# Kernel tuning notes

Measured on AMD Instinct MI355X. Metric: run time of the kernel, lower is better.

Reference implementation:

```python
import jax, jax.numpy as jnp
import numpy as np

PF = 16      # PATCH_FEATURES
PFD = 16     # PATCH_FEATURES_DEEP
NCLS = 10

def setup_inputs() -> dict:
    key = jax.random.key(0)
    ks = jax.random.split(key, 7)
    B = 131072
    x = jax.random.normal(ks[0], (B, 1, 28, 28), dtype=jnp.float32)
    # Linear params: W stored as [out, in] like torch, scaled kaiming-uniform-ish
    W1 = jax.random.uniform(ks[1], (PF, 49), jnp.float32, -1, 1) / jnp.sqrt(49.0)
    b1 = jax.random.uniform(ks[2], (PF,), jnp.float32, -1, 1) / jnp.sqrt(49.0)
    W2 = jax.random.uniform(ks[3], (PFD, 4 * PF), jnp.float32, -1, 1) / jnp.sqrt(64.0)
    b2 = jax.random.uniform(ks[4], (PFD,), jnp.float32, -1, 1) / jnp.sqrt(64.0)
    W3 = jax.random.uniform(ks[5], (NCLS, 4 * PFD), jnp.float32, -1, 1) / jnp.sqrt(64.0)
    b3 = jax.random.uniform(ks[6], (NCLS,), jnp.float32, -1, 1) / jnp.sqrt(64.0)
    return {"x": x, "W1": W1, "b1": b1, "W2": W2, "b2": b2, "W3": W3, "b3": b3}


def reference(x, W1, b1, W2, b2, W3, b3):
    # Dropout layers are identity in eval/inference mode.
    B = x.shape[0]
    img = x[:, 0]  # [B,28,28]
    # 16 non-overlapping 7x7 patches, flattened row-major (matches the torch slices)
    p = img.reshape(B, 4, 7, 4, 7).transpose(0, 1, 3, 2, 4).reshape(B, 4, 4, 49)
    # fc1 applied to every patch: one batched GEMM instead of 16 launches
    h = jnp.einsum('bijp,fp->bijf', p, W1) + b1          # [B,4,4,16]
    # group 2x2 patch blocks; concat order (x11,x12,x21,x22) = row-major (ii,jj)
    hb = h.reshape(B, 2, 2, 2, 2, PF).transpose(0, 1, 3, 2, 4, 5).reshape(B, 2, 2, 4 * PF)
    y = jnp.einsum('bijp,fp->bijf', hb, W2) + b2         # [B,2,2,16]
    # concat (y11,y12,y21,y22) row-major over (bi,bj), relu, fc3
    yflat = jax.nn.relu(y).reshape(B, 4 * PFD)           # [B,64]
    z = yflat @ W3.T + b3                                # [B,10]
    return jax.nn.log_softmax(z, axis=1)
```

## Files before the change

### kernel.cpp

```cpp
#include <hip/hip_runtime.h>

typedef float f32x4 __attribute__((ext_vector_type(4)));
typedef short bf16x8 __attribute__((ext_vector_type(8)));

#define XS 464
#define WOFF 29696
#define YOFF 29696
#define YS 144
#define BOFF 38912

__device__ __forceinline__ unsigned short f2bf(float f) {
  unsigned u = __builtin_bit_cast(unsigned, f);
  u += 0x7FFFu + ((u >> 16) & 1u);
  return (unsigned short)(u >> 16);
}
__device__ __forceinline__ unsigned packbf2(float a, float b) {
  return (unsigned)f2bf(a) | ((unsigned)f2bf(b) << 16);
}

__global__ __launch_bounds__(256, 2) void mnist_mfma(
    const float* __restrict__ x, const float* __restrict__ W1,
    const float* __restrict__ b1, const float* __restrict__ W2,
    const float* __restrict__ b2, const float* __restrict__ W3,
    const float* __restrict__ b3, float* __restrict__ out, int nimg)
{
  __shared__ __align__(16) char smem[38976];
  float* smemF = (float*)smem;
  const int tid = threadIdx.x;
  const int lane = tid & 63;
  const int waveid = tid >> 6;

  for (int i = tid; i < 784; i += 256) smemF[i] = W1[i];
  for (int i = tid; i < 1024; i += 256) smemF[784 + i] = W2[i];
  __syncthreads();

  unsigned short* w12b = (unsigned short*)(smem + WOFF);
  for (int e = tid; e < 3136; e += 256) {
    int f2 = e / 196, k = e - f2 * 196;
    int r14 = k / 14, c14 = k - r14 * 14;
    int pp = (r14 % 7) * 7 + (c14 % 7);
    int q = (r14 / 7) * 2 + (c14 / 7);
    float s = 0.f;
#pragma unroll
    for (int f = 0; f < 16; ++f)
      s = fmaf(smemF[f * 49 + pp], smemF[784 + f2 * 64 + q * 16 + f], s);
    w12b[f2 * 232 + k] = f2bf(s);
  }
  for (int e = tid; e < 576; e += 256) {
    int f2 = e / 36;
    w12b[f2 * 232 + 196 + (e - f2 * 36)] = 0;
  }
  if (tid < 16) {
    float s = b2[tid];
#pragma unroll
    for (int k = 0; k < 64; ++k)
      s = fmaf(b1[k & 15], smemF[784 + tid * 64 + k], s);
    smemF[BOFF / 4 + tid] = s;
  }
  __syncthreads();

  bf16x8 wfrag[7];
#pragma unroll
  for (int i = 0; i < 7; ++i)
    wfrag[i] = *(const bf16x8*)(smem + WOFF + (lane & 15) * XS + (lane >> 4) * 16 + i * 64);

  bf16x8 w3f[2];
  {
    int o = lane & 15, kb = (lane >> 4) * 8;
#pragma unroll
    for (int mi = 0; mi < 2; ++mi) {
      float v[8];
#pragma unroll
      for (int j = 0; j < 8; ++j)
        v[j] = (o < 10) ? W3[o * 64 + kb + 32 * mi + j] : 0.f;
      unsigned t[4];
      t[0] = packbf2(v[0], v[1]); t[1] = packbf2(v[2], v[3]);
      t[2] = packbf2(v[4], v[5]); t[3] = packbf2(v[6], v[7]);
      w3f[mi] = __builtin_bit_cast(bf16x8, *(unsigned(*)[4])t);
    }
  }
  const float b12v = smemF[BOFF / 4 + (lane & 15)];
  float b3v[4];
#pragma unroll
  for (int r = 0; r < 4; ++r) {
    int o = (lane >> 4) * 4 + r;
    b3v[r] = (o < 10) ? b3[o] : 0.f;
  }
  __syncthreads();

  char* xw = smem + waveid * 7424;
#pragma unroll
  for (int j = 0; j < 5; ++j) {
    int idx = lane + 64 * j;
    if (idx < 288) {
      int row = idx / 18, d = idx - row * 18;
      *(unsigned*)(xw + row * XS + 392 + d * 4) = 0;
    }
  }

  unsigned wa0[13]; unsigned strm = 0;
#pragma unroll
  for (int it = 0; it < 13; ++it) {
    int gi = lane + 64 * it;
    int im = gi / 196, rem = gi - im * 196;
    int rr = rem / 7, t = rem - rr * 7;
    int c2 = 2 * t;
    int J = c2 / 7, cq = c2 - 7 * J;
    int row = im * 4 + (rr / 14) * 2 + J;
    int kp = (rr % 14) * 7 + cq;
    wa0[it] = waveid * 7424 + row * XS + kp * 4;
    if (t == 3) strm |= (1u << it);
  }

  const unsigned xrd = waveid * 7424 + (lane & 15) * XS + (lane >> 4) * 16;
  const unsigned ywb = YOFF + waveid * 2304 + (lane & 15) * 2;
  const unsigned yrd = YOFF + waveid * 2304 + (lane & 15) * YS + (lane >> 4) * 16;

  const int NU = nimg >> 4;
  const int WST = (int)(gridDim.x << 2);
  const int w0 = (int)(blockIdx.x << 2) + waveid;
  const int ng4 = nimg >> 2;

  f32x4 cur[13];
  const f32x4* __restrict__ xq0 = (const f32x4*)x;
  auto issue4 = [&](int g4) {
    const f32x4* p = xq0 + (size_t)g4 * 784;
#pragma unroll
    for (int it = 0; it < 12; ++it)
      cur[it] = __builtin_nontemporal_load(p + lane + 64 * it);
    if (lane < 16) cur[12] = __builtin_nontemporal_load(p + 768 + lane);
  };

  if (w0 < NU) issue4(w0 * 4);

  for (int u = w0; u < NU; u += WST) {
#pragma unroll 1
    for (int sb = 0; sb < 4; ++sb) {
#pragma unroll
      for (int it = 0; it < 13; ++it) {
        if (it == 12 && lane >= 16) continue;
        f32x4 v = cur[it];
        unsigned a0 = wa0[it];
        unsigned d = ((strm >> it) & 1) ? 440u : 4u;
        *(unsigned*)(smem + a0) = packbf2(v.x, v.y);
        *(unsigned*)(smem + a0 + d) = packbf2(v.z, v.w);
      }
      int ng = (sb < 3) ? (u * 4 + sb + 1) : ((u + WST) * 4);
      if (ng < ng4) issue4(ng);
      f32x4 acc = {0.f, 0.f, 0.f, 0.f};
#pragma unroll
      for (int i = 0; i < 7; ++i) {
        bf16x8 a = *(const bf16x8*)(smem + xrd + 64 * i);
        acc = __builtin_amdgcn_mfma_f32_16x16x32_bf16(a, wfrag[i], acc, 0, 0, 0);
      }
      unsigned yb = ywb + (unsigned)(sb * 4 + (lane >> 4)) * YS;
#pragma unroll
      for (int r = 0; r < 4; ++r) {
        float yv = fmaxf(acc[r] + b12v, 0.f);
        *(unsigned short*)(smem + yb + r * 32) = f2bf(yv);
      }
    }
    f32x4 z4 = {0.f, 0.f, 0.f, 0.f};
#pragma unroll
    for (int mi = 0; mi < 2; ++mi) {
      bf16x8 bfr = *(const bf16x8*)(smem + yrd + 64 * mi);
      z4 = __builtin_amdgcn_mfma_f32_16x16x32_bf16(w3f[mi], bfr, z4, 0, 0, 0);
    }
    float zv[4], mval = -3.0e38f;
#pragma unroll
    for (int r = 0; r < 4; ++r) {
      zv[r] = z4[r] + b3v[r];
      bool valid = ((lane >> 4) * 4 + r) < 10;
      mval = fmaxf(mval, valid ? zv[r] : -3.0e38f);
    }
    mval = fmaxf(mval, __shfl_xor(mval, 16, 64));
    mval = fmaxf(mval, __shfl_xor(mval, 32, 64));
    float ssum = 0.f;
#pragma unroll
    for (int r = 0; r < 4; ++r) {
      bool valid = ((lane >> 4) * 4 + r) < 10;
      ssum += valid ? __expf(zv[r] - mval) : 0.f;
    }
    ssum += __shfl_xor(ssum, 16, 64);
    ssum += __shfl_xor(ssum, 32, 64);
    const float lse = mval + __logf(ssum);
    float* op = out + (size_t)(u * 16 + (lane & 15)) * 10;
#pragma unroll
    for (int r = 0; r < 4; ++r) {
      int o = (lane >> 4) * 4 + r;
      if (o < 10) op[o] = zv[r] - lse;
    }
  }
}

extern "C" void kernel_launch(void* const* d_in, const int* in_sizes, int n_in,
                              void* d_out, int out_size, void* d_ws, size_t ws_size,
                              hipStream_t stream) {
  const float* x  = (const float*)d_in[0];
  const float* W1 = (const float*)d_in[1];
  const float* b1 = (const float*)d_in[2];
  const float* W2 = (const float*)d_in[3];
  const float* b2 = (const float*)d_in[4];
  const float* W3 = (const float*)d_in[5];
  const float* b3 = (const float*)d_in[6];
  float* out = (float*)d_out;

  const int nimg = in_sizes[0] / 784;
  mnist_mfma<<<1024, 256, 0, stream>>>(x, W1, b1, W2, b2, W3, b3, out, nimg);
}
```

Before: 75.13 us.

## Double-buffer global image loads in registers to deepen the prefetch

Adds a second register buffer for input tiles, so two image groups' loads are in flight while the current group is staged to LDS and run through the MFMA. The loop is unrolled over two units per stride, alternating between the A and B buffers, and the next-next group is issued after each stage. The min-blocks hint is dropped from the launch bounds so the compiler can use the extra VGPRs. The intent is to hide more HBM latency in this bandwidth-bound kernel, at the cost of more registers and possibly lower occupancy.

```diff
diff --git a/kernel.cpp b/kernel.cpp
--- a/kernel.cpp
+++ b/kernel.cpp
@@ -18,7 +18,7 @@
   return (unsigned)f2bf(a) | ((unsigned)f2bf(b) << 16);
 }
 
-__global__ __launch_bounds__(256, 2) void mnist_mfma(
+__global__ __launch_bounds__(256) void mnist_mfma(
     const float* __restrict__ x, const float* __restrict__ W1,
     const float* __restrict__ b1, const float* __restrict__ W2,
     const float* __restrict__ b2, const float* __restrict__ W3,
@@ -119,47 +119,42 @@
   const int NU = nimg >> 4;
   const int WST = (int)(gridDim.x << 2);
   const int w0 = (int)(blockIdx.x << 2) + waveid;
-  const int ng4 = nimg >> 2;
-
-  f32x4 cur[13];
+
+  f32x4 curA[13], curB[13];
   const f32x4* __restrict__ xq0 = (const f32x4*)x;
-  auto issue4 = [&](int g4) {
+  auto issue4 = [&](f32x4 (&cur)[13], int g4) {
     const f32x4* p = xq0 + (size_t)g4 * 784;
 #pragma unroll
     for (int it = 0; it < 12; ++it)
       cur[it] = __builtin_nontemporal_load(p + lane + 64 * it);
     if (lane < 16) cur[12] = __builtin_nontemporal_load(p + 768 + lane);
   };
-
-  if (w0 < NU) issue4(w0 * 4);
-
-  for (int u = w0; u < NU; u += WST) {
-#pragma unroll 1
-    for (int sb = 0; sb < 4; ++sb) {
-#pragma unroll
-      for (int it = 0; it < 13; ++it) {
-        if (it == 12 && lane >= 16) continue;
-        f32x4 v = cur[it];
-        unsigned a0 = wa0[it];
-        unsigned d = ((strm >> it) & 1) ? 440u : 4u;
-        *(unsigned*)(smem + a0) = packbf2(v.x, v.y);
-        *(unsigned*)(smem + a0 + d) = packbf2(v.z, v.w);
-      }
-      int ng = (sb < 3) ? (u * 4 + sb + 1) : ((u + WST) * 4);
-      if (ng < ng4) issue4(ng);
-      f32x4 acc = {0.f, 0.f, 0.f, 0.f};
-#pragma unroll
-      for (int i = 0; i < 7; ++i) {
-        bf16x8 a = *(const bf16x8*)(smem + xrd + 64 * i);
-        acc = __builtin_amdgcn_mfma_f32_16x16x32_bf16(a, wfrag[i], acc, 0, 0, 0);
-      }
-      unsigned yb = ywb + (unsigned)(sb * 4 + (lane >> 4)) * YS;
-#pragma unroll
-      for (int r = 0; r < 4; ++r) {
-        float yv = fmaxf(acc[r] + b12v, 0.f);
-        *(unsigned short*)(smem + yb + r * 32) = f2bf(yv);
-      }
-    }
+  auto stage = [&](f32x4 (&cur)[13]) {
+#pragma unroll
+    for (int it = 0; it < 13; ++it) {
+      if (it == 12 && lane >= 16) continue;
+      f32x4 v = cur[it];
+      unsigned a0 = wa0[it];
+      unsigned d = ((strm >> it) & 1) ? 440u : 4u;
+      *(unsigned*)(smem + a0) = packbf2(v.x, v.y);
+      *(unsigned*)(smem + a0 + d) = packbf2(v.z, v.w);
+    }
+  };
+  auto gemm1 = [&](int sb) {
+    f32x4 acc = {0.f, 0.f, 0.f, 0.f};
+#pragma unroll
+    for (int i = 0; i < 7; ++i) {
+      bf16x8 a = *(const bf16x8*)(smem + xrd + 64 * i);
+      acc = __builtin_amdgcn_mfma_f32_16x16x32_bf16(a, wfrag[i], acc, 0, 0, 0);
+    }
+    unsigned yb = ywb + (unsigned)(sb * 4 + (lane >> 4)) * YS;
+#pragma unroll
+    for (int r = 0; r < 4; ++r) {
+      float yv = fmaxf(acc[r] + b12v, 0.f);
+      *(unsigned short*)(smem + yb + r * 32) = f2bf(yv);
+    }
+  };
+  auto epilogue = [&](int u) {
     f32x4 z4 = {0.f, 0.f, 0.f, 0.f};
 #pragma unroll
     for (int mi = 0; mi < 2; ++mi) {
@@ -189,6 +184,34 @@
     for (int r = 0; r < 4; ++r) {
       int o = (lane >> 4) * 4 + r;
       if (o < 10) op[o] = zv[r] - lse;
+    }
+  };
+
+  const int WST2 = WST * 2;
+  auto unitOf = [&](int u0, int j) { return u0 + (j >> 2) * WST; };
+
+  if (w0 < NU) {
+    issue4(curA, w0 * 4);
+    issue4(curB, w0 * 4 + 1);
+  }
+
+  for (int u0 = w0; u0 < NU; u0 += WST2) {
+#pragma unroll
+    for (int i = 0; i < 8; i += 2) {
+      if (unitOf(u0, i) < NU) {
+        stage(curA);
+        int ja = i + 2, ua = unitOf(u0, ja);
+        if (ua < NU) issue4(curA, ua * 4 + (ja & 3));
+        gemm1(i & 3);
+        if ((i & 3) == 3) epilogue(unitOf(u0, i));
+      }
+      if (unitOf(u0, i + 1) < NU) {
+        stage(curB);
+        int jb = i + 3, ub2 = unitOf(u0, jb);
+        if (ub2 < NU) issue4(curB, ub2 * 4 + (jb & 3));
+        gemm1((i + 1) & 3);
+        if (((i + 1) & 3) == 3) epilogue(unitOf(u0, i + 1));
+      }
     }
   }
 }
```

Measured after the change: 77.96 us. 1.04x slower.
